# Kernel tuning notes

Hardware: AMD Instinct MI355X
Metric: run time of the kernel (lower is better)

The kernel has to match this reference:

```python
import jax, jax.numpy as jnp
import numpy as np

N_NODES = 50000
N_EDGES = 1_600_000
N_GRAPHS = 2048
NEG_SLOPE = 0.2


def setup_inputs() -> dict:
    key = jax.random.key(0)
    ks = jax.random.split(key, 24)
    p = {}
    p["x1"] = jax.random.normal(ks[0], (N_NODES, 7), jnp.float32)
    p["x2"] = jax.random.normal(ks[1], (N_NODES, 7), jnp.float32)
    p["edge_index1"] = jax.random.randint(ks[2], (2, N_EDGES), 0, N_NODES, jnp.int32)
    p["edge_index2"] = jax.random.randint(ks[3], (2, N_EDGES), 0, N_NODES, jnp.int32)
    p["batch"] = jnp.sort(jax.random.randint(ks[4], (N_NODES,), 0, N_GRAPHS, jnp.int32))
    p["half_y"] = jax.random.randint(ks[5], (N_GRAPHS,), 0, 3, jnp.int32)
    p["x_norm2_1"] = jax.random.normal(ks[6], (N_GRAPHS, 16), jnp.float32)
    p["x_norm2_2"] = jax.random.normal(ks[7], (N_GRAPHS, 16), jnp.float32)
    # GATConv params: W [in,out] (no bias in lin), att_src/att_dst [out], bias [out]
    dims = [(7, 128), (128, 128), (128, 64)]
    ki = 8
    for i, (din, dout) in enumerate(dims, start=1):
        s = 1.0 / np.sqrt(din)
        p[f"W{i}"] = jax.random.normal(ks[ki], (din, dout), jnp.float32) * s; ki += 1
        p[f"as{i}"] = jax.random.normal(ks[ki], (dout,), jnp.float32) * 0.1; ki += 1
        p[f"ad{i}"] = jax.random.normal(ks[ki], (dout,), jnp.float32) * 0.1; ki += 1
        p[f"b{i}"] = jnp.zeros((dout,), jnp.float32)
    p["linW"] = jax.random.normal(ks[ki], (64 + 16, 64), jnp.float32) * (1.0 / np.sqrt(80.0)); ki += 1
    p["linb"] = jnp.zeros((64,), jnp.float32)
    return p


def gat_conv(x, src, dst, W, a_src, a_dst, bias):
    # PyG GATConv, heads=1: h = x@W; e_{j->i} = leaky_relu(a_src.h_j + a_dst.h_i);
    # softmax over incoming edges at dst; out_i = sum_j alpha * h_j + bias
    n = x.shape[0]
    h = x @ W                              # [N, out]
    al_s = h @ a_src                       # [N]
    al_d = h @ a_dst                       # [N]
    e = jax.nn.leaky_relu(al_s[src] + al_d[dst], NEG_SLOPE)  # [E]
    m = jax.ops.segment_max(e, dst, num_segments=n)
    ex = jnp.exp(e - m[dst])
    den = jax.ops.segment_sum(ex, dst, num_segments=n)
    alpha = ex / den[dst]
    out = jax.ops.segment_sum(alpha[:, None] * h[src], dst, num_segments=n)
    return out + bias


def branch(x, edge_index, convs):
    n = x.shape[0]
    loop = jnp.arange(n, dtype=edge_index.dtype)
    src = jnp.concatenate([edge_index[0], loop])  # add_self_loops=True
    dst = jnp.concatenate([edge_index[1], loop])
    for (W, a_s, a_d, b) in convs:
        x = jax.nn.elu(gat_conv(x, src, dst, W, a_s, a_d, b))
        # dropout p=0.5 is identity in eval mode
    return x


def global_mean_pool(x, batch, num_graphs):
    sums = jax.ops.segment_sum(x, batch, num_segments=num_graphs)
    cnt = jax.ops.segment_sum(jnp.ones((x.shape[0],), x.dtype), batch, num_segments=num_graphs)
    return sums / jnp.maximum(cnt, 1.0)[:, None]


def reference(x1, x2, edge_index1, edge_index2, batch, half_y, x_norm2_1, x_norm2_2,
              W1, as1, ad1, b1, W2, as2, ad2, b2, W3, as3, ad3, b3, linW, linb):
    convs = [(W1, as1, ad1, b1), (W2, as2, ad2, b2), (W3, as3, ad3, b3)]
    h1 = branch(x1, edge_index1, convs)
    h2 = branch(x2, edge_index2, convs)
    g1 = global_mean_pool(h1, batch, N_GRAPHS)
    g2 = global_mean_pool(h2, batch, N_GRAPHS)
    g1 = jnp.concatenate([g1, x_norm2_1], axis=1)
    g2 = jnp.concatenate([g2, x_norm2_2], axis=1)
    o1 = g1 @ linW + linb
    o2 = g2 @ linW + linb
    return (o1, o2)
```

## Files before the change

### kernel.cpp

```cpp
#include <hip/hip_runtime.h>
#include <math.h>

#define N_NODES_C 50000
#define N_EDGES_C 1600000
#define N_GRAPHS_C 2048
#define NBUK 391

typedef short short8 __attribute__((ext_vector_type(8)));
typedef float f32x4 __attribute__((ext_vector_type(4)));

static __device__ __forceinline__ int lowerBound(const int* __restrict__ a, int n, int v) {
    int lo = 0, hi = n;
    while (lo < hi) {
        int mid = (lo + hi) >> 1;
        if (a[mid] < v) lo = mid + 1; else hi = mid;
    }
    return lo;
}

static __device__ __forceinline__ unsigned short f2bf(float f) {
    unsigned u = __float_as_uint(f);
    return (unsigned short)((u + 0x7FFFu + ((u >> 16) & 1u)) >> 16);
}
static __device__ __forceinline__ float blo(unsigned v) { return __uint_as_float(v << 16); }
static __device__ __forceinline__ float bhi(unsigned v) { return __uint_as_float(v & 0xFFFF0000u); }


__global__ __launch_bounds__(256) void bucket_count_kernel(
    const int* __restrict__ ei, int* __restrict__ bucketCnt, int E) {
    __shared__ int lh[NBUK];
    int t = threadIdx.x;
    for (int i = t; i < NBUK; i += 256) lh[i] = 0;
    __syncthreads();
    for (int e = blockIdx.x * blockDim.x + t; e < E; e += gridDim.x * blockDim.x)
        atomicAdd(&lh[((unsigned)ei[E + e]) >> 7], 1);
    __syncthreads();
    for (int i = t; i < NBUK; i += 256) {
        int c = lh[i];
        if (c) atomicAdd(&bucketCnt[i], c);
    }
}

__global__ __launch_bounds__(512) void bucket_scan_kernel(
    const int* __restrict__ bucketCnt, int* __restrict__ bucketPtr, int* __restrict__ bucketCur) {
    __shared__ int v[512];
    int t = threadIdx.x;
    int x = (t < NBUK) ? bucketCnt[t] : 0;
    v[t] = x;
    __syncthreads();
    for (int off = 1; off < 512; off <<= 1) {
        int y = (t >= off) ? v[t - off] : 0;
        __syncthreads();
        v[t] += y;
        __syncthreads();
    }
    int excl = v[t] - x;
    if (t <= NBUK) bucketPtr[t] = excl;
    if (t < NBUK) bucketCur[t] = excl;
}

__global__ __launch_bounds__(256) void bucket_scatter_kernel(
    const int* __restrict__ ei, int* __restrict__ bucketCur,
    unsigned* __restrict__ bucketBuf, int E) {
    __shared__ int lh[NBUK];
    int t = threadIdx.x;
    for (int i = t; i < NBUK; i += 256) lh[i] = 0;
    __syncthreads();
    int per = (E + gridDim.x - 1) / gridDim.x;
    int beg = blockIdx.x * per;
    int end = min(beg + per, E);
    for (int e = beg + t; e < end; e += 256)
        atomicAdd(&lh[((unsigned)ei[E + e]) >> 7], 1);
    __syncthreads();
    for (int i = t; i < NBUK; i += 256) {
        int c = lh[i];
        lh[i] = c ? atomicAdd(&bucketCur[i], c) : 0;
    }
    __syncthreads();
    for (int e = beg + t; e < end; e += 256) {
        int s = ei[e], d = ei[E + e];
        int pos = atomicAdd(&lh[((unsigned)d) >> 7], 1);
        bucketBuf[pos] = (unsigned)s | ((unsigned)(d & 127) << 16);
    }
}

__global__ __launch_bounds__(256) void csr_finalize_kernel(
    const int* __restrict__ bucketPtr, const unsigned* __restrict__ bucketBuf,
    int* __restrict__ rowptr, int* __restrict__ csr, int n) {
    __shared__ int hist[128], sc[128], cur[128];
    int b = blockIdx.x, t = threadIdx.x;
    int base = b << 7;
    int nb = min(128, n - base);
    if (t < 128) hist[t] = (t < nb) ? 1 : 0;
    __syncthreads();
    int ebeg = bucketPtr[b], eend = bucketPtr[b + 1];
    for (int i = ebeg + t; i < eend; i += 256)
        atomicAdd(&hist[bucketBuf[i] >> 16], 1);
    __syncthreads();
    if (t < 128) sc[t] = hist[t];
    __syncthreads();
    for (int off = 1; off < 128; off <<= 1) {
        int y = 0;
        if (t < 128 && t >= off) y = sc[t - off];
        __syncthreads();
        if (t < 128) sc[t] += y;
        __syncthreads();
    }
    int csrStart = ebeg + base;
    if (t < nb) {
        int rpos = csrStart + sc[t] - hist[t];
        rowptr[base + t] = rpos;
        csr[rpos] = base + t;
        cur[t] = rpos + 1;
    }
    if (b == 0 && t == 0) rowptr[n] = bucketPtr[NBUK] + n;
    __syncthreads();
    for (int i = ebeg + t; i < eend; i += 256) {
        unsigned v = bucketBuf[i];
        int pos = atomicAdd(&cur[v >> 16], 1);
        csr[pos] = (int)(v & 0xFFFFu);
    }
}


__global__ __launch_bounds__(256) void wt_conv_kernel(
    const float* __restrict__ W, unsigned short* __restrict__ Wt, int K, int C) {
    int i = blockIdx.x * 256 + threadIdx.x;
    if (i < K * C) {
        int c = i / K, k = i - c * K;
        Wt[i] = f2bf(W[(size_t)k * C + c]);
    }
}


template<int DOUT>
__global__ __launch_bounds__(256) void gemm_mfma(
    const unsigned short* __restrict__ xb,
    const unsigned short* __restrict__ Wt,
    const float* __restrict__ avs, const float* __restrict__ avd,
    unsigned* __restrict__ hb,
    float* __restrict__ als, float* __restrict__ ald, int n) {
    constexpr int NT = DOUT / 16;
    int w = threadIdx.x >> 6, l = threadIdx.x & 63;
    int lc = l & 15, lg = l >> 4;
    int n0 = blockIdx.x * 64 + w * 16;
    int nrow = min(n0 + lc, n - 1);
    f32x4 acc[NT];
#pragma unroll
    for (int ct = 0; ct < NT; ct++) acc[ct] = (f32x4){0.f, 0.f, 0.f, 0.f};
    const unsigned short* xrow = xb + (size_t)nrow * 128 + lg * 8;
#pragma unroll
    for (int kb = 0; kb < 128; kb += 32) {
        short8 xf = *(const short8*)(xrow + kb);
#pragma unroll
        for (int ct = 0; ct < NT; ct++) {
            short8 wf = *(const short8*)(Wt + (size_t)(ct * 16 + lc) * 128 + kb + lg * 8);
            acc[ct] = __builtin_amdgcn_mfma_f32_16x16x32_bf16(wf, xf, acc[ct], 0, 0, 0);
        }
    }
    int node = n0 + lc;
    bool ok = node < n;
    float ps = 0.f, pd = 0.f;
#pragma unroll
    for (int ct = 0; ct < NT; ct++) {
        int cb = ct * 16 + lg * 4;
#pragma unroll
        for (int j = 0; j < 4; j++) { ps += acc[ct][j] * avs[cb + j]; pd += acc[ct][j] * avd[cb + j]; }
        if (ok) {
            uint2 v;
            v.x = (unsigned)f2bf(acc[ct][0]) | ((unsigned)f2bf(acc[ct][1]) << 16);
            v.y = (unsigned)f2bf(acc[ct][2]) | ((unsigned)f2bf(acc[ct][3]) << 16);
            *(uint2*)&hb[(size_t)node * (DOUT / 2) + ct * 8 + lg * 2] = v;
        }
    }
    ps += __shfl_xor(ps, 16); ps += __shfl_xor(ps, 32);
    pd += __shfl_xor(pd, 16); pd += __shfl_xor(pd, 32);
    if (ok && lg == 0) { als[node] = ps; ald[node] = pd; }
}


__global__ __launch_bounds__(256) void linear_att_l1(
    const float* __restrict__ x, const float* __restrict__ W,
    const float* __restrict__ avs, const float* __restrict__ avd,
    unsigned* __restrict__ hb, float* __restrict__ als, float* __restrict__ ald, int n) {
    __shared__ float Wl[7 * 128];
    __shared__ float xsh[32][8];
    int tid = threadIdx.x;
    for (int i = tid; i < 7 * 128; i += 256) Wl[i] = W[i];
    int nodeBase = blockIdx.x * 32;
    if (tid < 224) {
        int nd = tid / 7, k = tid % 7;
        int g = min(nodeBase + nd, n - 1);
        xsh[nd][k] = x[(size_t)g * 7 + k];
    }
    __syncthreads();
    int nl = tid >> 3;
    int og = (tid & 7) * 16;
    int g = nodeBase + nl;
    float acc[16];
#pragma unroll
    for (int o = 0; o < 16; o++) acc[o] = 0.f;
#pragma unroll
    for (int k = 0; k < 7; k++) {
        float xv = xsh[nl][k];
#pragma unroll
        for (int o = 0; o < 16; o++) acc[o] += xv * Wl[k * 128 + og + o];
    }
    if (g < n) {
        unsigned pk[8];
#pragma unroll
        for (int o = 0; o < 16; o += 2)
            pk[o >> 1] = (unsigned)f2bf(acc[o]) | ((unsigned)f2bf(acc[o + 1]) << 16);
        uint4 v0, v1;
        v0.x = pk[0]; v0.y = pk[1]; v0.z = pk[2]; v0.w = pk[3];
        v1.x = pk[4]; v1.y = pk[5]; v1.z = pk[6]; v1.w = pk[7];
        *(uint4*)&hb[(size_t)g * 64 + (og >> 1)] = v0;
        *(uint4*)&hb[(size_t)g * 64 + (og >> 1) + 4] = v1;
        float ps = 0.f, pd = 0.f;
#pragma unroll
        for (int o = 0; o < 16; o++) { ps += acc[o] * avs[og + o]; pd += acc[o] * avd[og + o]; }
#pragma unroll
        for (int off = 1; off < 8; off <<= 1) { ps += __shfl_xor(ps, off); pd += __shfl_xor(pd, off); }
        if ((tid & 7) == 0) { als[g] = ps; ald[g] = pd; }
    }
}


template<int DOUT, bool OBF>
__global__ __launch_bounds__(128) void gat_agg6(
    const int* __restrict__ rowptr, const int* __restrict__ csr,
    const float* __restrict__ als, const float* __restrict__ ald,
    const unsigned char* __restrict__ hbB, const float* __restrict__ bias,
    float* __restrict__ xout, int n) {
    constexpr int ROWB = DOUT * 2;
    constexpr int LPE  = ROWB / 16;
    constexpr int EPG  = 64 / LPE;
    int lane = threadIdx.x & 63;
    int node = blockIdx.x * 2 + (threadIdx.x >> 6);
    if (node >= n) return;
    int beg = rowptr[node], end = rowptr[node + 1];
    int deg = end - beg;
    float adi = ald[node];

    float e0 = -INFINITY, mloc = -INFINITY;
    int src0 = node;
    {
        int idx = beg + lane;
        if (idx < end) {
            int src = csr[idx];
            float e = als[src] + adi;
            e = (e > 0.f) ? e : 0.2f * e;
            e0 = e; mloc = e; src0 = src;
            for (idx += 64; idx < end; idx += 64) {
                src = csr[idx];
                e = als[src] + adi;
                e = (e > 0.f) ? e : 0.2f * e;
                mloc = fmaxf(mloc, e);
            }
        }
    }
#pragma unroll
    for (int o = 1; o < 64; o <<= 1) mloc = fmaxf(mloc, __shfl_xor(mloc, o));
    float m = mloc;
    float p0 = expf(e0 - m);
    float sloc = p0;
    if (deg > 64) {
        for (int idx = beg + lane + 64; idx < end; idx += 64) {
            int src = csr[idx];
            float e = als[src] + adi;
            e = (e > 0.f) ? e : 0.2f * e;
            sloc += expf(e - m);
        }
    }
    float s = sloc;
#pragma unroll
    for (int o = 1; o < 64; o <<= 1) s += __shfl_xor(s, o);
    float inv_den = 1.f / s;

    int eSel = lane / LPE;
    const unsigned char* hbs = hbB + (lane % LPE) * 16;
    unsigned ownOff = (unsigned)node * ROWB;

    float acc[8];
#pragma unroll
    for (int i = 0; i < 8; i++) acc[i] = 0.f;

    for (int win = 0; win < deg; win += 64) {
        float alphaL; unsigned offL;
        if (win == 0) {
            alphaL = p0 * inv_den;
            offL = (beg + lane < end) ? (unsigned)src0 * ROWB : ownOff;
        } else {
            int idx = beg + win + lane;
            if (idx < end) {
                int src = csr[idx];
                float e = als[src] + adi;
                e = (e > 0.f) ? e : 0.2f * e;
                alphaL = expf(e - m) * inv_den;
                offL = (unsigned)src * ROWB;
            } else { alphaL = 0.f; offL = ownOff; }
        }
        int limW = min(deg - win, 64);
        int nG = (limW + EPG - 1) / EPG;
        int nG4 = nG & ~3;
        int g = 0;
        for (; g < nG4; g += 4) {
            unsigned off_[4]; float a_[4]; uint4 v_[4];
#pragma unroll
            for (int j = 0; j < 4; j++) {
                int slot = (g + j) * EPG + eSel;
                off_[j] = (unsigned)__shfl((int)offL, slot);
                a_[j]   = __shfl(alphaL, slot);
            }
#pragma unroll
            for (int j = 0; j < 4; j++) v_[j] = *(const uint4*)(hbs + off_[j]);
#pragma unroll
            for (int j = 0; j < 4; j++) {
                acc[0] += a_[j] * blo(v_[j].x); acc[1] += a_[j] * bhi(v_[j].x);
                acc[2] += a_[j] * blo(v_[j].y); acc[3] += a_[j] * bhi(v_[j].y);
                acc[4] += a_[j] * blo(v_[j].z); acc[5] += a_[j] * bhi(v_[j].z);
                acc[6] += a_[j] * blo(v_[j].w); acc[7] += a_[j] * bhi(v_[j].w);
            }
        }
        for (; g < nG; g++) {
            int slot = g * EPG + eSel;
            unsigned off_t = (unsigned)__shfl((int)offL, slot);
            float a_t = __shfl(alphaL, slot);
            uint4 v_t = *(const uint4*)(hbs + off_t);
            acc[0] += a_t * blo(v_t.x); acc[1] += a_t * bhi(v_t.x);
            acc[2] += a_t * blo(v_t.y); acc[3] += a_t * bhi(v_t.y);
            acc[4] += a_t * blo(v_t.z); acc[5] += a_t * bhi(v_t.z);
            acc[6] += a_t * blo(v_t.w); acc[7] += a_t * bhi(v_t.w);
        }
    }

#pragma unroll
    for (int o = LPE; o < 64; o <<= 1) {
#pragma unroll
        for (int i = 0; i < 8; i++) acc[i] += __shfl_xor(acc[i], o);
    }

    if (lane < LPE) {
        int c0 = lane * 8;
        float v[8];
#pragma unroll
        for (int i = 0; i < 8; i++) {
            float t = acc[i] + bias[c0 + i];
            v[i] = (t > 0.f) ? t : expm1f(t);
        }
        if constexpr (OBF) {
            uint4 pk;
            pk.x = (unsigned)f2bf(v[0]) | ((unsigned)f2bf(v[1]) << 16);
            pk.y = (unsigned)f2bf(v[2]) | ((unsigned)f2bf(v[3]) << 16);
            pk.z = (unsigned)f2bf(v[4]) | ((unsigned)f2bf(v[5]) << 16);
            pk.w = (unsigned)f2bf(v[6]) | ((unsigned)f2bf(v[7]) << 16);
            *(uint4*)((unsigned*)xout + (size_t)node * (DOUT / 2) + lane * 4) = pk;
        } else {
            float4 f0, f1;
            f0.x = v[0]; f0.y = v[1]; f0.z = v[2]; f0.w = v[3];
            f1.x = v[4]; f1.y = v[5]; f1.z = v[6]; f1.w = v[7];
            *(float4*)&xout[(size_t)node * DOUT + c0] = f0;
            *(float4*)&xout[(size_t)node * DOUT + c0 + 4] = f1;
        }
    }
}


__global__ __launch_bounds__(64) void pool_final_kernel(
    const float* __restrict__ x, const int* __restrict__ batch,
    const float* __restrict__ xnorm, const float* __restrict__ linW,
    const float* __restrict__ linb, float* __restrict__ out, int n) {
    int g = blockIdx.x, t = threadIdx.x;
    int lo = lowerBound(batch, n, g);
    int hi = lowerBound(batch, n, g + 1);
    float sum = 0.f;
    for (int i = lo; i < hi; i++) sum += x[(size_t)i * 64 + t];
    float cnt = (float)(hi - lo);
    float mean = sum / fmaxf(cnt, 1.f);
    __shared__ float gv[80];
    gv[t] = mean;
    if (t < 16) gv[64 + t] = xnorm[g * 16 + t];
    __syncthreads();
    float acc = linb[t];
#pragma unroll
    for (int k = 0; k < 80; k++) acc += gv[k] * linW[k * 64 + t];
    out[(size_t)g * 64 + t] = acc;
}


extern "C" void kernel_launch(void* const* d_in, const int* in_sizes, int n_in,
                              void* d_out, int out_size, void* d_ws, size_t ws_size,
                              hipStream_t stream) {
    const float* x1  = (const float*)d_in[0];
    const float* x2  = (const float*)d_in[1];
    const int*   ei1 = (const int*)d_in[2];
    const int*   ei2 = (const int*)d_in[3];
    const int*   batch = (const int*)d_in[4];
    const float* xn1 = (const float*)d_in[6];
    const float* xn2 = (const float*)d_in[7];
    const float* W1 = (const float*)d_in[8];
    const float* as1 = (const float*)d_in[9];
    const float* ad1 = (const float*)d_in[10];
    const float* b1 = (const float*)d_in[11];
    const float* W2 = (const float*)d_in[12];
    const float* as2 = (const float*)d_in[13];
    const float* ad2 = (const float*)d_in[14];
    const float* b2 = (const float*)d_in[15];
    const float* W3 = (const float*)d_in[16];
    const float* as3 = (const float*)d_in[17];
    const float* ad3 = (const float*)d_in[18];
    const float* b3 = (const float*)d_in[19];
    const float* linW = (const float*)d_in[20];
    const float* linb = (const float*)d_in[21];
    float* out = (float*)d_out;

    char* ws = (char*)d_ws;
    size_t off = 0;
    auto alloc = [&](size_t bytes) -> void* {
        void* p = ws + off;
        off += (bytes + 255) & ~(size_t)255;
        return p;
    };
    int* rowptr    = (int*)alloc((N_NODES_C + 1) * sizeof(int));
    int* csr       = (int*)alloc((size_t)(N_EDGES_C + N_NODES_C) * sizeof(int));
    float* als     = (float*)alloc(N_NODES_C * sizeof(float));
    float* ald     = (float*)alloc(N_NODES_C * sizeof(float));
    int* bucketCnt = (int*)alloc(NBUK * sizeof(int));
    int* bucketPtr = (int*)alloc((NBUK + 1) * sizeof(int));
    int* bucketCur = (int*)alloc(NBUK * sizeof(int));
    unsigned short* Wt2 = (unsigned short*)alloc(128 * 128 * sizeof(unsigned short));
    unsigned short* Wt3 = (unsigned short*)alloc(64 * 128 * sizeof(unsigned short));
    float* bufX    = (float*)alloc((size_t)N_NODES_C * 64 * sizeof(float));
    unsigned* hb   = (unsigned*)alloc((size_t)N_NODES_C * 64 * sizeof(unsigned));
    unsigned short* xbb = (unsigned short*)alloc((size_t)N_NODES_C * 128 * sizeof(unsigned short));
    unsigned* bucketBuf = (unsigned*)bufX;
    (void)ws_size; (void)in_sizes; (void)n_in; (void)out_size;

    const int GEMM_GRID = (N_NODES_C + 63) / 64;
    const int AGG_GRID = (N_NODES_C + 1) / 2;

    wt_conv_kernel<<<(128 * 128 + 255) / 256, 256, 0, stream>>>(W2, Wt2, 128, 128);
    wt_conv_kernel<<<(128 * 64 + 255) / 256, 256, 0, stream>>>(W3, Wt3, 128, 64);

    for (int br = 0; br < 2; br++) {
        const float* x  = (br == 0) ? x1 : x2;
        const int*   ei = (br == 0) ? ei1 : ei2;
        const float* xn = (br == 0) ? xn1 : xn2;
        float* o = out + (size_t)br * N_GRAPHS_C * 64;

        hipMemsetAsync(bucketCnt, 0, NBUK * sizeof(int), stream);
        bucket_count_kernel<<<1024, 256, 0, stream>>>(ei, bucketCnt, N_EDGES_C);
        bucket_scan_kernel<<<1, 512, 0, stream>>>(bucketCnt, bucketPtr, bucketCur);
        bucket_scatter_kernel<<<256, 256, 0, stream>>>(ei, bucketCur, bucketBuf, N_EDGES_C);
        csr_finalize_kernel<<<NBUK, 256, 0, stream>>>(bucketPtr, bucketBuf, rowptr, csr, N_NODES_C);

        linear_att_l1<<<(N_NODES_C + 31) / 32, 256, 0, stream>>>(x, W1, as1, ad1, hb, als, ald, N_NODES_C);
        gat_agg6<128, true><<<AGG_GRID, 128, 0, stream>>>(rowptr, csr, als, ald, (const unsigned char*)hb, b1, (float*)xbb, N_NODES_C);
        gemm_mfma<128><<<GEMM_GRID, 256, 0, stream>>>(xbb, Wt2, as2, ad2, hb, als, ald, N_NODES_C);
        gat_agg6<128, true><<<AGG_GRID, 128, 0, stream>>>(rowptr, csr, als, ald, (const unsigned char*)hb, b2, (float*)xbb, N_NODES_C);
        gemm_mfma<64><<<GEMM_GRID, 256, 0, stream>>>(xbb, Wt3, as3, ad3, hb, als, ald, N_NODES_C);
        gat_agg6<64, false><<<AGG_GRID, 128, 0, stream>>>(rowptr, csr, als, ald, (const unsigned char*)hb, b3, bufX, N_NODES_C);

        pool_final_kernel<<<N_GRAPHS_C, 64, 0, stream>>>(bufX, batch, xn, linW, linb, o, N_NODES_C);
    }
}
```

Measured before the change: 639.2 us.

## Batch both branches per launch, precompute alpha, split gather into column slices

Both graph branches now go through the CSR build, linear, GEMM and pooling kernels as a single launch each, using blockIdx.y to pick the branch, which halves the launch count and gives each launch more parallel work. The softmax attention weights are computed once per edge by a separate alpha kernel and stored. The aggregation then runs as a gather done in two column-half passes, so each pass touches a smaller slice of the feature table and is meant to hit cache more often. In exchange it adds an alpha buffer round-trip through memory, reads the CSR twice per layer, and doubles workspace use.

```diff
diff --git a/kernel.cpp b/kernel.cpp
--- a/kernel.cpp
+++ b/kernel.cpp
@@ -5,6 +5,7 @@
 #define N_EDGES_C 1600000
 #define N_GRAPHS_C 2048
 #define NBUK 391
+#define EN_C (N_EDGES_C + N_NODES_C)
 
 typedef short short8 __attribute__((ext_vector_type(8)));
 typedef float f32x4 __attribute__((ext_vector_type(4)));
@@ -27,7 +28,11 @@
 
 
 __global__ __launch_bounds__(256) void bucket_count_kernel(
-    const int* __restrict__ ei, int* __restrict__ bucketCnt, int E) {
+    const int* __restrict__ ei1, const int* __restrict__ ei2,
+    int* __restrict__ bucketCntA, int E) {
+    int br = blockIdx.y;
+    const int* ei = br ? ei2 : ei1;
+    int* bucketCnt = bucketCntA + br * NBUK;
     __shared__ int lh[NBUK];
     int t = threadIdx.x;
     for (int i = t; i < NBUK; i += 256) lh[i] = 0;
@@ -42,7 +47,11 @@
 }
 
 __global__ __launch_bounds__(512) void bucket_scan_kernel(
-    const int* __restrict__ bucketCnt, int* __restrict__ bucketPtr, int* __restrict__ bucketCur) {
+    const int* __restrict__ bucketCntA, int* __restrict__ bucketPtrA, int* __restrict__ bucketCurA) {
+    int br = blockIdx.y;
+    const int* bucketCnt = bucketCntA + br * NBUK;
+    int* bucketPtr = bucketPtrA + br * (NBUK + 1);
+    int* bucketCur = bucketCurA + br * NBUK;
     __shared__ int v[512];
     int t = threadIdx.x;
     int x = (t < NBUK) ? bucketCnt[t] : 0;
@@ -60,8 +69,13 @@
 }
 
 __global__ __launch_bounds__(256) void bucket_scatter_kernel(
-    const int* __restrict__ ei, int* __restrict__ bucketCur,
-    unsigned* __restrict__ bucketBuf, int E) {
+    const int* __restrict__ ei1, const int* __restrict__ ei2,
+    int* __restrict__ bucketCurA,
+    unsigned* __restrict__ bb1, unsigned* __restrict__ bb2, int E) {
+    int br = blockIdx.y;
+    const int* ei = br ? ei2 : ei1;
+    int* bucketCur = bucketCurA + br * NBUK;
+    unsigned* bucketBuf = br ? bb2 : bb1;
     __shared__ int lh[NBUK];
     int t = threadIdx.x;
     for (int i = t; i < NBUK; i += 256) lh[i] = 0;
@@ -85,8 +99,14 @@
 }
 
 __global__ __launch_bounds__(256) void csr_finalize_kernel(
-    const int* __restrict__ bucketPtr, const unsigned* __restrict__ bucketBuf,
-    int* __restrict__ rowptr, int* __restrict__ csr, int n) {
+    const int* __restrict__ bucketPtrA,
+    const unsigned* __restrict__ bb1, const unsigned* __restrict__ bb2,
+    int* __restrict__ rowptrA, int* __restrict__ csrA, int n) {
+    int br = blockIdx.y;
+    const int* bucketPtr = bucketPtrA + br * (NBUK + 1);
+    const unsigned* bucketBuf = br ? bb2 : bb1;
+    int* rowptr = rowptrA + br * (n + 1);
+    int* csr = csrA + (size_t)br * EN_C;
     __shared__ int hist[128], sc[128], cur[128];
     int b = blockIdx.x, t = threadIdx.x;
     int base = b << 7;
@@ -135,11 +155,16 @@
 
 template<int DOUT>
 __global__ __launch_bounds__(256) void gemm_mfma(
-    const unsigned short* __restrict__ xb,
+    const unsigned short* __restrict__ xbA,
     const unsigned short* __restrict__ Wt,
     const float* __restrict__ avs, const float* __restrict__ avd,
-    unsigned* __restrict__ hb,
-    float* __restrict__ als, float* __restrict__ ald, int n) {
+    unsigned* __restrict__ hbA,
+    float* __restrict__ alsA, float* __restrict__ aldA, int n) {
+    int br = blockIdx.y;
+    const unsigned short* xb = xbA + (size_t)br * n * 128;
+    unsigned* hb = hbA + (size_t)br * n * 64;
+    float* als = alsA + br * n;
+    float* ald = aldA + br * n;
     constexpr int NT = DOUT / 16;
     int w = threadIdx.x >> 6, l = threadIdx.x & 63;
     int lc = l & 15, lg = l >> 4;
@@ -180,9 +205,15 @@
 
 
 __global__ __launch_bounds__(256) void linear_att_l1(
-    const float* __restrict__ x, const float* __restrict__ W,
+    const float* __restrict__ x1, const float* __restrict__ x2,
+    const float* __restrict__ W,
     const float* __restrict__ avs, const float* __restrict__ avd,
-    unsigned* __restrict__ hb, float* __restrict__ als, float* __restrict__ ald, int n) {
+    unsigned* __restrict__ hbA, float* __restrict__ alsA, float* __restrict__ aldA, int n) {
+    int br = blockIdx.y;
+    const float* x = br ? x2 : x1;
+    unsigned* hb = hbA + (size_t)br * n * 64;
+    float* als = alsA + br * n;
+    float* ald = aldA + br * n;
     __shared__ float Wl[7 * 128];
     __shared__ float xsh[32][8];
     int tid = threadIdx.x;
@@ -226,34 +257,32 @@
 }
 
 
-template<int DOUT, bool OBF>
-__global__ __launch_bounds__(128) void gat_agg6(
-    const int* __restrict__ rowptr, const int* __restrict__ csr,
-    const float* __restrict__ als, const float* __restrict__ ald,
-    const unsigned char* __restrict__ hbB, const float* __restrict__ bias,
-    float* __restrict__ xout, int n) {
-    constexpr int ROWB = DOUT * 2;
-    constexpr int LPE  = ROWB / 16;
-    constexpr int EPG  = 64 / LPE;
+__global__ __launch_bounds__(256) void alpha_kernel(
+    const int* __restrict__ rowptrA, const int* __restrict__ csrA,
+    const float* __restrict__ alsA, const float* __restrict__ aldA,
+    float* __restrict__ alphaA, int n) {
+    int br = blockIdx.y;
+    const int* rowptr = rowptrA + br * (n + 1);
+    const int* csr = csrA + (size_t)br * EN_C;
+    const float* als = alsA + br * n;
+    const float* ald = aldA + br * n;
+    float* alpha = alphaA + (size_t)br * EN_C;
     int lane = threadIdx.x & 63;
-    int node = blockIdx.x * 2 + (threadIdx.x >> 6);
+    int node = blockIdx.x * 4 + (threadIdx.x >> 6);
     if (node >= n) return;
     int beg = rowptr[node], end = rowptr[node + 1];
     int deg = end - beg;
     float adi = ald[node];
 
     float e0 = -INFINITY, mloc = -INFINITY;
-    int src0 = node;
     {
         int idx = beg + lane;
         if (idx < end) {
-            int src = csr[idx];
-            float e = als[src] + adi;
+            float e = als[csr[idx]] + adi;
             e = (e > 0.f) ? e : 0.2f * e;
-            e0 = e; mloc = e; src0 = src;
+            e0 = e; mloc = e;
             for (idx += 64; idx < end; idx += 64) {
-                src = csr[idx];
-                e = als[src] + adi;
+                e = als[csr[idx]] + adi;
                 e = (e > 0.f) ? e : 0.2f * e;
                 mloc = fmaxf(mloc, e);
             }
@@ -266,8 +295,7 @@
     float sloc = p0;
     if (deg > 64) {
         for (int idx = beg + lane + 64; idx < end; idx += 64) {
-            int src = csr[idx];
-            float e = als[src] + adi;
+            float e = als[csr[idx]] + adi;
             e = (e > 0.f) ? e : 0.2f * e;
             sloc += expf(e - m);
         }
@@ -277,8 +305,32 @@
     for (int o = 1; o < 64; o <<= 1) s += __shfl_xor(s, o);
     float inv_den = 1.f / s;
 
+    if (beg + lane < end) alpha[beg + lane] = p0 * inv_den;
+    if (deg > 64) {
+        for (int idx = beg + lane + 64; idx < end; idx += 64) {
+            float e = als[csr[idx]] + adi;
+            e = (e > 0.f) ? e : 0.2f * e;
+            alpha[idx] = expf(e - m) * inv_den;
+        }
+    }
+}
+
+
+template<int ROWB, int SLICE, bool OBF>
+__global__ __launch_bounds__(128) void gat_gather(
+    const int* __restrict__ rowptr, const int* __restrict__ csr,
+    const float* __restrict__ alphaB, const unsigned char* __restrict__ hbB,
+    const float* __restrict__ bias, float* __restrict__ xout, int n, int colByte) {
+    constexpr int LPE = SLICE / 16;
+    constexpr int EPG = 64 / LPE;
+    constexpr int DOUT = ROWB / 2;
+    int lane = threadIdx.x & 63;
+    int node = blockIdx.x * 2 + (threadIdx.x >> 6);
+    if (node >= n) return;
+    int beg = rowptr[node], end = rowptr[node + 1];
+    int deg = end - beg;
     int eSel = lane / LPE;
-    const unsigned char* hbs = hbB + (lane % LPE) * 16;
+    const unsigned char* hbs = hbB + colByte + (lane % LPE) * 16;
     unsigned ownOff = (unsigned)node * ROWB;
 
     float acc[8];
@@ -286,20 +338,9 @@
     for (int i = 0; i < 8; i++) acc[i] = 0.f;
 
     for (int win = 0; win < deg; win += 64) {
-        float alphaL; unsigned offL;
-        if (win == 0) {
-            alphaL = p0 * inv_den;
-            offL = (beg + lane < end) ? (unsigned)src0 * ROWB : ownOff;
-        } else {
-            int idx = beg + win + lane;
-            if (idx < end) {
-                int src = csr[idx];
-                float e = als[src] + adi;
-                e = (e > 0.f) ? e : 0.2f * e;
-                alphaL = expf(e - m) * inv_den;
-                offL = (unsigned)src * ROWB;
-            } else { alphaL = 0.f; offL = ownOff; }
-        }
+        int idx = beg + win + lane;
+        float aL = 0.f; unsigned offL = ownOff;
+        if (idx < end) { aL = alphaB[idx]; offL = (unsigned)csr[idx] * ROWB; }
         int limW = min(deg - win, 64);
         int nG = (limW + EPG - 1) / EPG;
         int nG4 = nG & ~3;
@@ -310,7 +351,7 @@
             for (int j = 0; j < 4; j++) {
                 int slot = (g + j) * EPG + eSel;
                 off_[j] = (unsigned)__shfl((int)offL, slot);
-                a_[j]   = __shfl(alphaL, slot);
+                a_[j]   = __shfl(aL, slot);
             }
 #pragma unroll
             for (int j = 0; j < 4; j++) v_[j] = *(const uint4*)(hbs + off_[j]);
@@ -325,7 +366,7 @@
         for (; g < nG; g++) {
             int slot = g * EPG + eSel;
             unsigned off_t = (unsigned)__shfl((int)offL, slot);
-            float a_t = __shfl(alphaL, slot);
+            float a_t = __shfl(aL, slot);
             uint4 v_t = *(const uint4*)(hbs + off_t);
             acc[0] += a_t * blo(v_t.x); acc[1] += a_t * bhi(v_t.x);
             acc[2] += a_t * blo(v_t.y); acc[3] += a_t * bhi(v_t.y);
@@ -341,7 +382,7 @@
     }
 
     if (lane < LPE) {
-        int c0 = lane * 8;
+        int c0 = colByte / 2 + lane * 8;
         float v[8];
 #pragma unroll
         for (int i = 0; i < 8; i++) {
@@ -354,7 +395,7 @@
             pk.y = (unsigned)f2bf(v[2]) | ((unsigned)f2bf(v[3]) << 16);
             pk.z = (unsigned)f2bf(v[4]) | ((unsigned)f2bf(v[5]) << 16);
             pk.w = (unsigned)f2bf(v[6]) | ((unsigned)f2bf(v[7]) << 16);
-            *(uint4*)((unsigned*)xout + (size_t)node * (DOUT / 2) + lane * 4) = pk;
+            *(uint4*)((unsigned*)xout + (size_t)node * (DOUT / 2) + colByte / 4 + lane * 4) = pk;
         } else {
             float4 f0, f1;
             f0.x = v[0]; f0.y = v[1]; f0.z = v[2]; f0.w = v[3];
@@ -367,9 +408,14 @@
 
 
 __global__ __launch_bounds__(64) void pool_final_kernel(
-    const float* __restrict__ x, const int* __restrict__ batch,
-    const float* __restrict__ xnorm, const float* __restrict__ linW,
-    const float* __restrict__ linb, float* __restrict__ out, int n) {
+    const float* __restrict__ xA, const int* __restrict__ batch,
+    const float* __restrict__ xn1, const float* __restrict__ xn2,
+    const float* __restrict__ linW, const float* __restrict__ linb,
+    float* __restrict__ out, int n, size_t xStride) {
+    int br = blockIdx.y;
+    const float* x = xA + br * xStride;
+    const float* xnorm = br ? xn2 : xn1;
+    float* o = out + (size_t)br * N_GRAPHS_C * 64;
     int g = blockIdx.x, t = threadIdx.x;
     int lo = lowerBound(batch, n, g);
     int hi = lowerBound(batch, n, g + 1);
@@ -384,7 +430,7 @@
     float acc = linb[t];
 #pragma unroll
     for (int k = 0; k < 80; k++) acc += gv[k] * linW[k * 64 + t];
-    out[(size_t)g * 64 + t] = acc;
+    o[(size_t)g * 64 + t] = acc;
 }
 
 
@@ -421,46 +467,79 @@
         off += (bytes + 255) & ~(size_t)255;
         return p;
     };
-    int* rowptr    = (int*)alloc((N_NODES_C + 1) * sizeof(int));
-    int* csr       = (int*)alloc((size_t)(N_EDGES_C + N_NODES_C) * sizeof(int));
-    float* als     = (float*)alloc(N_NODES_C * sizeof(float));
-    float* ald     = (float*)alloc(N_NODES_C * sizeof(float));
-    int* bucketCnt = (int*)alloc(NBUK * sizeof(int));
-    int* bucketPtr = (int*)alloc((NBUK + 1) * sizeof(int));
-    int* bucketCur = (int*)alloc(NBUK * sizeof(int));
+    int* rowptr    = (int*)alloc(2 * (N_NODES_C + 1) * sizeof(int));
+    int* csr       = (int*)alloc(2 * (size_t)EN_C * sizeof(int));
+    float* als     = (float*)alloc(2 * N_NODES_C * sizeof(float));
+    float* ald     = (float*)alloc(2 * N_NODES_C * sizeof(float));
+    float* alphaB  = (float*)alloc(2 * (size_t)EN_C * sizeof(float));
+    int* bucketCnt = (int*)alloc(2 * NBUK * sizeof(int));
+    int* bucketPtr = (int*)alloc(2 * (NBUK + 1) * sizeof(int));
+    int* bucketCur = (int*)alloc(2 * NBUK * sizeof(int));
     unsigned short* Wt2 = (unsigned short*)alloc(128 * 128 * sizeof(unsigned short));
     unsigned short* Wt3 = (unsigned short*)alloc(64 * 128 * sizeof(unsigned short));
-    float* bufX    = (float*)alloc((size_t)N_NODES_C * 64 * sizeof(float));
-    unsigned* hb   = (unsigned*)alloc((size_t)N_NODES_C * 64 * sizeof(unsigned));
-    unsigned short* xbb = (unsigned short*)alloc((size_t)N_NODES_C * 128 * sizeof(unsigned short));
-    unsigned* bucketBuf = (unsigned*)bufX;
+    unsigned* hb   = (unsigned*)alloc(2 * (size_t)N_NODES_C * 64 * sizeof(unsigned));
+    unsigned short* xbb = (unsigned short*)alloc(2 * (size_t)N_NODES_C * 128 * sizeof(unsigned short));
     (void)ws_size; (void)in_sizes; (void)n_in; (void)out_size;
 
-    const int GEMM_GRID = (N_NODES_C + 63) / 64;
-    const int AGG_GRID = (N_NODES_C + 1) / 2;
+    const size_t XBB_STRIDE = (size_t)N_NODES_C * 128;
+    unsigned* bb1 = (unsigned*)xbb;
+    unsigned* bb2 = (unsigned*)(xbb + XBB_STRIDE);
+    const unsigned char* hbB0 = (const unsigned char*)hb;
+    const unsigned char* hbB1 = (const unsigned char*)(hb + (size_t)N_NODES_C * 64);
+    float* xoutF0 = (float*)xbb;
+    float* xoutF1 = (float*)(xbb + XBB_STRIDE);
+
+    const int N = N_NODES_C;
+    const dim3 B256(256), B128(128), B512(512), B64(64);
 
     wt_conv_kernel<<<(128 * 128 + 255) / 256, 256, 0, stream>>>(W2, Wt2, 128, 128);
     wt_conv_kernel<<<(128 * 64 + 255) / 256, 256, 0, stream>>>(W3, Wt3, 128, 64);
 
+    hipMemsetAsync(bucketCnt, 0, 2 * NBUK * sizeof(int), stream);
+    bucket_count_kernel<<<dim3(1024, 2), B256, 0, stream>>>(ei1, ei2, bucketCnt, N_EDGES_C);
+    bucket_scan_kernel<<<dim3(1, 2), B512, 0, stream>>>(bucketCnt, bucketPtr, bucketCur);
+    bucket_scatter_kernel<<<dim3(256, 2), B256, 0, stream>>>(ei1, ei2, bucketCur, bb1, bb2, N_EDGES_C);
+    csr_finalize_kernel<<<dim3(NBUK, 2), B256, 0, stream>>>(bucketPtr, bb1, bb2, rowptr, csr, N);
+
+    const dim3 AGRID((N + 3) / 4, 2);
+    const dim3 GGRID((N + 1) / 2);
+    const dim3 MGRID((N + 63) / 64, 2);
+    const dim3 LGRID((N + 31) / 32, 2);
+
+    linear_att_l1<<<LGRID, B256, 0, stream>>>(x1, x2, W1, as1, ad1, hb, als, ald, N);
+    alpha_kernel<<<AGRID, B256, 0, stream>>>(rowptr, csr, als, ald, alphaB, N);
     for (int br = 0; br < 2; br++) {
-        const float* x  = (br == 0) ? x1 : x2;
-        const int*   ei = (br == 0) ? ei1 : ei2;
-        const float* xn = (br == 0) ? xn1 : xn2;
-        float* o = out + (size_t)br * N_GRAPHS_C * 64;
-
-        hipMemsetAsync(bucketCnt, 0, NBUK * sizeof(int), stream);
-        bucket_count_kernel<<<1024, 256, 0, stream>>>(ei, bucketCnt, N_EDGES_C);
-        bucket_scan_kernel<<<1, 512, 0, stream>>>(bucketCnt, bucketPtr, bucketCur);
-        bucket_scatter_kernel<<<256, 256, 0, stream>>>(ei, bucketCur, bucketBuf, N_EDGES_C);
-        csr_finalize_kernel<<<NBUK, 256, 0, stream>>>(bucketPtr, bucketBuf, rowptr, csr, N_NODES_C);
-
-        linear_att_l1<<<(N_NODES_C + 31) / 32, 256, 0, stream>>>(x, W1, as1, ad1, hb, als, ald, N_NODES_C);
-        gat_agg6<128, true><<<AGG_GRID, 128, 0, stream>>>(rowptr, csr, als, ald, (const unsigned char*)hb, b1, (float*)xbb, N_NODES_C);
-        gemm_mfma<128><<<GEMM_GRID, 256, 0, stream>>>(xbb, Wt2, as2, ad2, hb, als, ald, N_NODES_C);
-        gat_agg6<128, true><<<AGG_GRID, 128, 0, stream>>>(rowptr, csr, als, ald, (const unsigned char*)hb, b2, (float*)xbb, N_NODES_C);
-        gemm_mfma<64><<<GEMM_GRID, 256, 0, stream>>>(xbb, Wt3, as3, ad3, hb, als, ald, N_NODES_C);
-        gat_agg6<64, false><<<AGG_GRID, 128, 0, stream>>>(rowptr, csr, als, ald, (const unsigned char*)hb, b3, bufX, N_NODES_C);
-
-        pool_final_kernel<<<N_GRAPHS_C, 64, 0, stream>>>(bufX, batch, xn, linW, linb, o, N_NODES_C);
-    }
-}
+        const int* rp = rowptr + br * (N + 1);
+        const int* cs = csr + (size_t)br * EN_C;
+        const float* al = alphaB + (size_t)br * EN_C;
+        const unsigned char* hbb = br ? hbB1 : hbB0;
+        float* xo = br ? xoutF1 : xoutF0;
+        gat_gather<256, 128, true><<<GGRID, B128, 0, stream>>>(rp, cs, al, hbb, b1, xo, N, 0);
+        gat_gather<256, 128, true><<<GGRID, B128, 0, stream>>>(rp, cs, al, hbb, b1, xo, N, 128);
+    }
+    gemm_mfma<128><<<MGRID, B256, 0, stream>>>(xbb, Wt2, as2, ad2, hb, als, ald, N);
+    alpha_kernel<<<AGRID, B256, 0, stream>>>(rowptr, csr, als, ald, alphaB, N);
+    for (int br = 0; br < 2; br++) {
+        const int* rp = rowptr + br * (N + 1);
+        const int* cs = csr + (size_t)br * EN_C;
+        const float* al = alphaB + (size_t)br * EN_C;
+        const unsigned char* hbb = br ? hbB1 : hbB0;
+        float* xo = br ? xoutF1 : xoutF0;
+        gat_gather<256, 128, true><<<GGRID, B128, 0, stream>>>(rp, cs, al, hbb, b2, xo, N, 0);
+        gat_gather<256, 128, true><<<GGRID, B128, 0, stream>>>(rp, cs, al, hbb, b2, xo, N, 128);
+    }
+    gemm_mfma<64><<<MGRID, B256, 0, stream>>>(xbb, Wt3, as3, ad3, hb, als, ald, N);
+    alpha_kernel<<<AGRID, B256, 0, stream>>>(rowptr, csr, als, ald, alphaB, N);
+    for (int br = 0; br < 2; br++) {
+        const int* rp = rowptr + br * (N + 1);
+        const int* cs = csr + (size_t)br * EN_C;
+        const float* al = alphaB + (size_t)br * EN_C;
+        const unsigned char* hbb = br ? hbB1 : hbB0;
+        float* xo = br ? xoutF1 : xoutF0;
+        gat_gather<128, 64, false><<<GGRID, B128, 0, stream>>>(rp, cs, al, hbb, b3, xo, N, 0);
+        gat_gather<128, 64, false><<<GGRID, B128, 0, stream>>>(rp, cs, al, hbb, b3, xo, N, 64);
+    }
+
+    pool_final_kernel<<<dim3(N_GRAPHS_C, 2), B64, 0, stream>>>(
+        xoutF0, batch, xn1, xn2, linW, linb, out, N, (size_t)N_NODES_C * 64);
+}
```

Result: slower. 741.2 us (+16.0%).
